# Kernel tuning notes

Hardware: AMD Instinct MI355X
Metric: run time of the kernel (lower is better)

## Reference

```python
import jax, jax.numpy as jnp
import numpy as np
import math

HEADS = 8
EMBED = 512
HEAD_DIM = EMBED // HEADS
N, L = 2, 256


def setup_inputs() -> dict:
    key = jax.random.key(0)
    ks = jax.random.split(key, 16)
    s = 0.05  # weight scale for numerical stability
    inp = {
        "values": jax.random.normal(ks[0], (N, L, EMBED), jnp.float32),
        "keys": jax.random.normal(ks[1], (N, L, EMBED), jnp.float32),
        "query": jax.random.normal(ks[2], (N, L, EMBED), jnp.float32),
        "pos": jax.random.normal(ks[3], (N, L, EMBED), jnp.float32),
        "rel": jax.random.normal(ks[4], (N, L, L, EMBED), jnp.float32),
        "mask": jnp.ones((N, L), jnp.float32),
        "Wv": jax.random.normal(ks[5], (HEAD_DIM, HEAD_DIM), jnp.float32) * s,
        "Wk": jax.random.normal(ks[6], (HEAD_DIM, HEAD_DIM), jnp.float32) * s,
        "Wq": jax.random.normal(ks[7], (HEAD_DIM, HEAD_DIM), jnp.float32) * s,
        "Wpq": jax.random.normal(ks[8], (HEAD_DIM, HEAD_DIM), jnp.float32) * s,
        "Wpk": jax.random.normal(ks[9], (HEAD_DIM, HEAD_DIM), jnp.float32) * s,
        "Wrk": jax.random.normal(ks[10], (HEAD_DIM, HEAD_DIM), jnp.float32) * s,
        "Wrq": jax.random.normal(ks[11], (HEAD_DIM, HEAD_DIM), jnp.float32) * s,
        "Wout": jax.random.normal(ks[12], (EMBED, EMBED), jnp.float32) * s,
        "bout": jnp.zeros((EMBED,), jnp.float32),
    }
    return inp


def reference(values, keys, query, pos, rel, mask, Wv, Wk, Wq, Wpq, Wpk, Wrk, Wrq, Wout, bout):
    n, lq, e = query.shape
    h, d = HEADS, e // HEADS
    # split heads; per-head Linear shares one [d,d] weight (y = x @ W.T)
    v = values.reshape(n, -1, h, d) @ Wv.T
    k = keys.reshape(n, -1, h, d) @ Wk.T
    q = query.reshape(n, lq, h, d) @ Wq.T
    p = pos.reshape(n, lq, h, d)
    r = rel.reshape(n, lq, lq, h, d)
    # mode == 'all': QK + pos-pos + two relative terms
    scores = jnp.einsum('nqhd,nkhd->nhqk', q, k)
    pq = p @ Wpq.T
    pk = p @ Wpk.T
    pos_scores = jnp.einsum('nqhd,nkhd->nhqk', pq, pk)
    rk = r @ Wrk.T
    rq = r @ Wrq.T
    rel1 = jnp.einsum('nqhd,nqkhd->nhqk', q, rk)
    rel2 = jnp.einsum('nqkhd,nkhd->nhqk', rq, k)
    energy = (scores + pos_scores + rel1 + rel2) / math.sqrt(2.0)
    energy = energy + (1.0 - mask)[:, None, None, :] * (-1e9)
    attn = jax.nn.softmax(energy, axis=3)
    out = jnp.einsum('nhqk,nkhd->nqhd', attn, v).reshape(n, lq, e)
    return out @ Wout.T + bout
```

## Files before the change

kernel.cpp:

```cpp
#include <hip/hip_runtime.h>
#include <hip/hip_bf16.h>

#define NB 2
#define L 256
#define H 8
#define D 64
#define E 512
#define NL (NB * L)
#define RSQRT2 0.70710678118654752f

__global__ __launch_bounds__(256) void k0_transpose(
    const float* __restrict__ Wout, float* __restrict__ WoutT,
    const float* __restrict__ Wq, const float* __restrict__ Wk,
    const float* __restrict__ Wv, const float* __restrict__ Wpq,
    const float* __restrict__ Wpk,
    float* __restrict__ WqT, float* __restrict__ WkT, float* __restrict__ WvT,
    float* __restrict__ WpqT, float* __restrict__ WpkT) {
    __shared__ float tile[64][65];
    int t = threadIdx.x;
    int tx = t & 63, ty = t >> 6;
    if (blockIdx.x < 64) {
        int bi = blockIdx.x >> 3;
        int bj = blockIdx.x & 7;
#pragma unroll
        for (int m = 0; m < 16; m++) {
            int el = ty + (m << 2);
            tile[el][tx] = Wout[(size_t)(bi * 64 + el) * E + bj * 64 + tx];
        }
        __syncthreads();
#pragma unroll
        for (int m = 0; m < 16; m++) {
            int cl = ty + (m << 2);
            WoutT[(size_t)(bj * 64 + cl) * E + bi * 64 + tx] = tile[tx][cl];
        }
    } else {
        const float* src;
        float* dst;
        switch (blockIdx.x - 64) {
            case 0: src = Wq;  dst = WqT;  break;
            case 1: src = Wk;  dst = WkT;  break;
            case 2: src = Wv;  dst = WvT;  break;
            case 3: src = Wpq; dst = WpqT; break;
            default: src = Wpk; dst = WpkT; break;
        }
#pragma unroll
        for (int m = 0; m < 16; m++) {
            int r = ty + (m << 2);
            tile[r][tx] = src[(r << 6) + tx];
        }
        __syncthreads();
#pragma unroll
        for (int m = 0; m < 16; m++) {
            int r = ty + (m << 2);
            dst[(r << 6) + tx] = tile[tx][r];
        }
    }
}

__global__ __launch_bounds__(256) void k1_proj(
    const float* __restrict__ values, const float* __restrict__ keys,
    const float* __restrict__ query, const float* __restrict__ pos,
    const float* __restrict__ WqT, const float* __restrict__ WkT,
    const float* __restrict__ WvT, const float* __restrict__ WpqT,
    const float* __restrict__ WpkT, const float* __restrict__ Wrk,
    const float* __restrict__ Wrq,
    float* __restrict__ qv_ws, float* __restrict__ kv_ws,
    float* __restrict__ vv_ws, float* __restrict__ pq_ws,
    float* __restrict__ pk_ws, float* __restrict__ qrk_ws,
    float* __restrict__ krq_ws) {
    __shared__ float xq[E], xk[E], xv[E], xp[E];
    __shared__ float qs[E], ks[E];
    int t = threadIdx.x;
    int nl = blockIdx.x;
    size_t base = (size_t)nl * E;
    for (int j = t; j < E; j += 256) {
        xq[j] = query[base + j];
        xk[j] = keys[base + j];
        xv[j] = values[base + j];
        xp[j] = pos[base + j];
    }
    __syncthreads();
#pragma unroll
    for (int cc = 0; cc < 2; cc++) {
        int c = t + (cc << 8);
        int h = c >> 6, i = c & 63;
        const float* xqh = xq + (h << 6);
        const float* xkh = xk + (h << 6);
        const float* xvh = xv + (h << 6);
        const float* xph = xp + (h << 6);
        float q_c = 0.f, k_c = 0.f, v_c = 0.f, pq_c = 0.f, pk_c = 0.f;
#pragma unroll 8
        for (int j = 0; j < 64; j++) {
            int wi = (j << 6) + i;
            float xqj = xqh[j], xkj = xkh[j], xvj = xvh[j], xpj = xph[j];
            q_c = fmaf(xqj, WqT[wi], q_c);
            k_c = fmaf(xkj, WkT[wi], k_c);
            v_c = fmaf(xvj, WvT[wi], v_c);
            pq_c = fmaf(xpj, WpqT[wi], pq_c);
            pk_c = fmaf(xpj, WpkT[wi], pk_c);
        }
        qv_ws[base + c] = q_c;
        kv_ws[base + c] = k_c;
        vv_ws[base + c] = v_c;
        pq_ws[base + c] = pq_c;
        pk_ws[base + c] = pk_c;
        qs[c] = q_c;
        ks[c] = k_c;
    }
    __syncthreads();
#pragma unroll
    for (int cc = 0; cc < 2; cc++) {
        int c = t + (cc << 8);
        int h = c >> 6, d = c & 63;
        float aq = 0.f, ak = 0.f;
        const float* qh = qs + (h << 6);
        const float* kh = ks + (h << 6);
#pragma unroll 8
        for (int i = 0; i < 64; i++) {
            aq = fmaf(qh[i], Wrk[(i << 6) + d], aq);
            ak = fmaf(kh[i], Wrq[(i << 6) + d], ak);
        }
        qrk_ws[base + c] = aq;
        krq_ws[base + c] = ak;
    }
}

__global__ __launch_bounds__(256) void k2pre(
    const float* __restrict__ qv_ws, const float* __restrict__ kv_ws,
    const float* __restrict__ pq_ws, const float* __restrict__ pk_ws,
    const float* __restrict__ mask, float* __restrict__ e_ws) {
    __shared__ float qs[8 * 64], ps[8 * 64];
    int t = threadIdx.x;
    int b = blockIdx.x;
    int qt = b & 31;
    int h = (b >> 5) & 7;
    int n = b >> 8;
    int nb = n << 8;
    int q0 = qt << 3;
    int k = t;
#pragma unroll
    for (int it = 0; it < 2; it++) {
        int idx = t + (it << 8);
        int q = idx >> 6, d = idx & 63;
        size_t g = (size_t)(nb + q0 + q) * E + (h << 6) + d;
        qs[idx] = qv_ws[g];
        ps[idx] = pq_ws[g];
    }
    __syncthreads();
    const float4* kv4p = (const float4*)(kv_ws + (size_t)(nb + k) * E + (h << 6));
    const float4* pk4p = (const float4*)(pk_ws + (size_t)(nb + k) * E + (h << 6));
    float acc[8];
#pragma unroll
    for (int q = 0; q < 8; q++) acc[q] = 0.f;
#pragma unroll
    for (int d4 = 0; d4 < 16; d4++) {
        float4 kv4 = kv4p[d4];
        float4 pk4 = pk4p[d4];
#pragma unroll
        for (int q = 0; q < 8; q++) {
            float4 q4 = ((const float4*)qs)[(q << 4) + d4];
            float4 p4 = ((const float4*)ps)[(q << 4) + d4];
            float a = acc[q];
            a = fmaf(q4.x, kv4.x, a);
            a = fmaf(q4.y, kv4.y, a);
            a = fmaf(q4.z, kv4.z, a);
            a = fmaf(q4.w, kv4.w, a);
            a = fmaf(p4.x, pk4.x, a);
            a = fmaf(p4.y, pk4.y, a);
            a = fmaf(p4.z, pk4.z, a);
            a = fmaf(p4.w, pk4.w, a);
            acc[q] = a;
        }
    }
    float mk = (1.0f - mask[nb + k]) * (-1e9f);
#pragma unroll
    for (int q = 0; q < 8; q++) {
        e_ws[(size_t)(nb + q0 + q) * (H * L) + (h << 8) + k] = acc[q] * RSQRT2 + mk;
    }
}


#define K2F_LOAD(RR, RK, c_)                                              \
    do {                                                                  \
        _Pragma("unroll") for (int jj = 0; jj < 4; jj++) {                \
            int k_ = ((c_) << 3) + (jj << 1) + rowsel;                    \
            size_t o_ = ((size_t)k_ << 9) + cq;                           \
            RR[jj] = *(const float4*)(relb + o_);                         \
            RK[jj] = *(const float4*)(krqb + o_);                         \
        }                                                                 \
    } while (0)

#define K2F_COMP(RR, RK, c_)                                              \
    do {                                                                  \
        _Pragma("unroll") for (int jj = 0; jj < 4; jj++) {                \
            float wx = qrk4.x + RK[jj].x;                                 \
            float wy = qrk4.y + RK[jj].y;                                 \
            float wz = qrk4.z + RK[jj].z;                                 \
            float ww = qrk4.w + RK[jj].w;                                 \
            float p = RR[jj].x * wx;                                      \
            p = fmaf(RR[jj].y, wy, p);                                    \
            p = fmaf(RR[jj].z, wz, p);                                    \
            p = fmaf(RR[jj].w, ww, p);                                    \
            p += __shfl_down(p, 8, 16);                                   \
            p += __shfl_down(p, 4, 16);                                   \
            p += __shfl_down(p, 2, 16);                                   \
            p += __shfl_down(p, 1, 16);                                   \
            if (sub == 0) {                                               \
                int k_ = ((c_) << 3) + (jj << 1) + rowsel;                \
                r_s[(h << 8) + k_] = p * RSQRT2;                          \
            }                                                             \
        }                                                                 \
    } while (0)

__global__ __launch_bounds__(256, 2) void k2f(
    const float* __restrict__ rel, const float* __restrict__ qrk_ws,
    const float* __restrict__ krq_ws, const float* __restrict__ e_ws,
    const float* __restrict__ vv_ws, float* __restrict__ attn_ws) {
    __shared__ float e_s[H * L];
    __shared__ float r_s[H * L];
    __shared__ float PS[2 * E];
    __shared__ float inv_s[H];
    int t = threadIdx.x;
    int nq = blockIdx.x;
    int n = nq >> 8;

    {
        const float4* src = (const float4*)(e_ws + (size_t)nq * (H * L));
        ((float4*)e_s)[t] = src[t];
        ((float4*)e_s)[t + 256] = src[t + 256];
    }

    int lane128 = t & 127;
    int rowsel = t >> 7;
    int cq = lane128 << 2;
    int h = lane128 >> 4;
    int sub = t & 15;

    const float* relb = rel + (((size_t)nq) << 8) * E;
    const float* krqb = krq_ws + (((size_t)(n << 8))) * E;
    float4 qrk4 = *(const float4*)(qrk_ws + (size_t)nq * E + cq);

    float4 rAr[4], rAk[4], rBr[4], rBk[4];
    K2F_LOAD(rAr, rAk, 0);
#pragma unroll
    for (int c = 0; c < 32; c += 2) {
        K2F_LOAD(rBr, rBk, c + 1);
        K2F_COMP(rAr, rAk, c);
        if (c + 2 < 32) K2F_LOAD(rAr, rAk, c + 2);
        K2F_COMP(rBr, rBk, c + 1);
    }
    __syncthreads();

    {
        int hh = t >> 5;
        int l32 = t & 31;
        float* eh = e_s + (hh << 8);
        const float* rh = r_s + (hh << 8);
        float x[8];
        float m = -INFINITY;
#pragma unroll
        for (int j = 0; j < 8; j++) {
            int idx = l32 + (j << 5);
            x[j] = eh[idx] + rh[idx];
            m = fmaxf(m, x[j]);
        }
#pragma unroll
        for (int off = 16; off > 0; off >>= 1) m = fmaxf(m, __shfl_xor(m, off, 32));
        float s = 0.f;
#pragma unroll
        for (int j = 0; j < 8; j++) {
            int idx = l32 + (j << 5);
            float ev = __expf(x[j] - m);
            eh[idx] = ev;
            s += ev;
        }
#pragma unroll
        for (int off = 16; off > 0; off >>= 1) s += __shfl_xor(s, off, 32);
        if (l32 == 0) inv_s[hh] = 1.0f / s;
    }
    __syncthreads();

    {
        int c4 = (t & 127) << 2;
        int kseg = t >> 7;
        int h1 = c4 >> 6;
        const float* eh = e_s + (h1 << 8) + (kseg << 7);
        const float* vb = vv_ws + ((size_t)((n << 8) + (kseg << 7))) * E + c4;
        float4 acc = {0.f, 0.f, 0.f, 0.f};
#pragma unroll 16
        for (int k = 0; k < 128; k++) {
            float ev = eh[k];
            float4 v4 = *(const float4*)(vb + ((size_t)k << 9));
            acc.x = fmaf(ev, v4.x, acc.x);
            acc.y = fmaf(ev, v4.y, acc.y);
            acc.z = fmaf(ev, v4.z, acc.z);
            acc.w = fmaf(ev, v4.w, acc.w);
        }
        *(float4*)(PS + kseg * E + c4) = acc;
    }
    __syncthreads();

    {
        float v0 = PS[t] + PS[E + t];
        attn_ws[(size_t)nq * E + t] = v0 * inv_s[t >> 6];
        float v1 = PS[256 + t] + PS[E + 256 + t];
        attn_ws[(size_t)nq * E + 256 + t] = v1 * inv_s[(256 + t) >> 6];
    }
}

__global__ __launch_bounds__(512) void k3_out(const float* __restrict__ attn_ws,
                                              const float* __restrict__ WoutT,
                                              const float* __restrict__ bout,
                                              float* __restrict__ out) {
    __shared__ float As[4 * E];
    int t = threadIdx.x;
    int r0 = blockIdx.x << 2;
    for (int j = t; j < 4 * E; j += 512) As[j] = attn_ws[(size_t)r0 * E + j];
    __syncthreads();
    float b0 = bout[t];
    float a0 = b0, a1 = b0, a2 = b0, a3 = b0;
#pragma unroll 8
    for (int c = 0; c < E; c++) {
        float w = WoutT[((size_t)c << 9) + t];
        a0 = fmaf(As[c], w, a0);
        a1 = fmaf(As[E + c], w, a1);
        a2 = fmaf(As[2 * E + c], w, a2);
        a3 = fmaf(As[3 * E + c], w, a3);
    }
    out[(size_t)(r0 + 0) * E + t] = a0;
    out[(size_t)(r0 + 1) * E + t] = a1;
    out[(size_t)(r0 + 2) * E + t] = a2;
    out[(size_t)(r0 + 3) * E + t] = a3;
}

extern "C" void kernel_launch(void* const* d_in, const int* in_sizes, int n_in,
                              void* d_out, int out_size, void* d_ws, size_t ws_size,
                              hipStream_t stream) {
    const float* values = (const float*)d_in[0];
    const float* keys = (const float*)d_in[1];
    const float* query = (const float*)d_in[2];
    const float* pos = (const float*)d_in[3];
    const float* rel = (const float*)d_in[4];
    const float* mask = (const float*)d_in[5];
    const float* Wv = (const float*)d_in[6];
    const float* Wk = (const float*)d_in[7];
    const float* Wq = (const float*)d_in[8];
    const float* Wpq = (const float*)d_in[9];
    const float* Wpk = (const float*)d_in[10];
    const float* Wrk = (const float*)d_in[11];
    const float* Wrq = (const float*)d_in[12];
    const float* Wout = (const float*)d_in[13];
    const float* bout = (const float*)d_in[14];
    float* out = (float*)d_out;

    float* ws = (float*)d_ws;
    const size_t SZ = (size_t)NL * E;
    float* qv_ws = ws + 0 * SZ;
    float* kv_ws = ws + 1 * SZ;
    float* vv_ws = ws + 2 * SZ;
    float* pq_ws = ws + 3 * SZ;
    float* pk_ws = ws + 4 * SZ;
    float* qrk_ws = ws + 5 * SZ;
    float* krq_ws = ws + 6 * SZ;
    float* attn_ws = ws + 7 * SZ;
    float* WoutT = ws + 8 * SZ;
    float* e_ws = ws + 9 * SZ;
    float* WqT = e_ws + (size_t)NL * (H * L);
    float* WkT = WqT + 4096;
    float* WvT = WkT + 4096;
    float* WpqT = WvT + 4096;
    float* WpkT = WpqT + 4096;

    k0_transpose<<<69, 256, 0, stream>>>(Wout, WoutT, Wq, Wk, Wv, Wpq, Wpk,
                                         WqT, WkT, WvT, WpqT, WpkT);
    k1_proj<<<NL, 256, 0, stream>>>(values, keys, query, pos, WqT, WkT, WvT,
                                    WpqT, WpkT, Wrk, Wrq, qv_ws, kv_ws, vv_ws,
                                    pq_ws, pk_ws, qrk_ws, krq_ws);
    k2pre<<<512, 256, 0, stream>>>(qv_ws, kv_ws, pq_ws, pk_ws, mask, e_ws);
    k2f<<<512, 256, 0, stream>>>(rel, qrk_ws, krq_ws, e_ws, vv_ws, attn_ws);
    k3_out<<<NL / 4, 512, 0, stream>>>(attn_ws, WoutT, bout, out);
}
```

Baseline: 503.7 us.

## Register-block k1 projections over four outputs, two tokens per block; deepen k2f prefetch

k1_proj now handles two tokens per block. Each thread computes four adjacent output columns using float4 weight loads and padded LDS rows, which cuts the number of weight-load instructions and the block count by half. Separately, k2f's rel/krq prefetch buffers grow from 4 to 8 rows per stage, so more memory requests are in flight over the dominant rel stream. This raises register pressure in k2f (32 float4 buffers), which could spill or reduce occupancy under launch_bounds(256,2).

```diff
diff --git a/kernel.cpp b/kernel.cpp
--- a/kernel.cpp
+++ b/kernel.cpp
@@ -57,6 +57,8 @@
     }
 }
 
+#define XS 68
+
 __global__ __launch_bounds__(256) void k1_proj(
     const float* __restrict__ values, const float* __restrict__ keys,
     const float* __restrict__ query, const float* __restrict__ pos,
@@ -68,60 +70,98 @@
     float* __restrict__ vv_ws, float* __restrict__ pq_ws,
     float* __restrict__ pk_ws, float* __restrict__ qrk_ws,
     float* __restrict__ krq_ws) {
-    __shared__ float xq[E], xk[E], xv[E], xp[E];
-    __shared__ float qs[E], ks[E];
+    __shared__ float x_lds[4][2][8 * XS];
+    __shared__ float qk_lds[2][2][8 * XS];
     int t = threadIdx.x;
-    int nl = blockIdx.x;
-    size_t base = (size_t)nl * E;
-    for (int j = t; j < E; j += 256) {
-        xq[j] = query[base + j];
-        xk[j] = keys[base + j];
-        xv[j] = values[base + j];
-        xp[j] = pos[base + j];
-    }
-    __syncthreads();
-#pragma unroll
-    for (int cc = 0; cc < 2; cc++) {
-        int c = t + (cc << 8);
-        int h = c >> 6, i = c & 63;
-        const float* xqh = xq + (h << 6);
-        const float* xkh = xk + (h << 6);
-        const float* xvh = xv + (h << 6);
-        const float* xph = xp + (h << 6);
-        float q_c = 0.f, k_c = 0.f, v_c = 0.f, pq_c = 0.f, pk_c = 0.f;
+    int tok0 = blockIdx.x << 1;
+
+    {
+        int tk = t >> 7;
+        int quad = t & 127;
+        int hh = quad >> 4;
+        int li = quad & 15;
+        size_t g = (size_t)(tok0 + tk) * E + (quad << 2);
+        float4 vq = *(const float4*)(query + g);
+        float4 vk = *(const float4*)(keys + g);
+        float4 vv = *(const float4*)(values + g);
+        float4 vp = *(const float4*)(pos + g);
+        int o = hh * XS + (li << 2);
+        *(float4*)&x_lds[0][tk][o] = vq;
+        *(float4*)&x_lds[1][tk][o] = vk;
+        *(float4*)&x_lds[2][tk][o] = vv;
+        *(float4*)&x_lds[3][tk][o] = vp;
+    }
+    __syncthreads();
+
+    int tk = t >> 7;
+    int quad = t & 127;
+    int h = quad >> 4;
+    int li = quad & 15;
+    const float* xq = &x_lds[0][tk][h * XS];
+    const float* xk = &x_lds[1][tk][h * XS];
+    const float* xv = &x_lds[2][tk][h * XS];
+    const float* xp = &x_lds[3][tk][h * XS];
+    const float4* wq4 = (const float4*)WqT + li;
+    const float4* wk4 = (const float4*)WkT + li;
+    const float4* wv4 = (const float4*)WvT + li;
+    const float4* wpq4 = (const float4*)WpqT + li;
+    const float4* wpk4 = (const float4*)WpkT + li;
+
+    float4 aq = {0, 0, 0, 0}, ak = {0, 0, 0, 0}, av = {0, 0, 0, 0};
+    float4 apq = {0, 0, 0, 0}, apk = {0, 0, 0, 0};
 #pragma unroll 8
-        for (int j = 0; j < 64; j++) {
-            int wi = (j << 6) + i;
-            float xqj = xqh[j], xkj = xkh[j], xvj = xvh[j], xpj = xph[j];
-            q_c = fmaf(xqj, WqT[wi], q_c);
-            k_c = fmaf(xkj, WkT[wi], k_c);
-            v_c = fmaf(xvj, WvT[wi], v_c);
-            pq_c = fmaf(xpj, WpqT[wi], pq_c);
-            pk_c = fmaf(xpj, WpkT[wi], pk_c);
-        }
-        qv_ws[base + c] = q_c;
-        kv_ws[base + c] = k_c;
-        vv_ws[base + c] = v_c;
-        pq_ws[base + c] = pq_c;
-        pk_ws[base + c] = pk_c;
-        qs[c] = q_c;
-        ks[c] = k_c;
-    }
-    __syncthreads();
-#pragma unroll
-    for (int cc = 0; cc < 2; cc++) {
-        int c = t + (cc << 8);
-        int h = c >> 6, d = c & 63;
-        float aq = 0.f, ak = 0.f;
-        const float* qh = qs + (h << 6);
-        const float* kh = ks + (h << 6);
+    for (int j = 0; j < 64; j++) {
+        float xqj = xq[j], xkj = xk[j], xvj = xv[j], xpj = xp[j];
+        float4 w;
+        w = wq4[j << 4];
+        aq.x = fmaf(xqj, w.x, aq.x); aq.y = fmaf(xqj, w.y, aq.y);
+        aq.z = fmaf(xqj, w.z, aq.z); aq.w = fmaf(xqj, w.w, aq.w);
+        w = wk4[j << 4];
+        ak.x = fmaf(xkj, w.x, ak.x); ak.y = fmaf(xkj, w.y, ak.y);
+        ak.z = fmaf(xkj, w.z, ak.z); ak.w = fmaf(xkj, w.w, ak.w);
+        w = wv4[j << 4];
+        av.x = fmaf(xvj, w.x, av.x); av.y = fmaf(xvj, w.y, av.y);
+        av.z = fmaf(xvj, w.z, av.z); av.w = fmaf(xvj, w.w, av.w);
+        w = wpq4[j << 4];
+        apq.x = fmaf(xpj, w.x, apq.x); apq.y = fmaf(xpj, w.y, apq.y);
+        apq.z = fmaf(xpj, w.z, apq.z); apq.w = fmaf(xpj, w.w, apq.w);
+        w = wpk4[j << 4];
+        apk.x = fmaf(xpj, w.x, apk.x); apk.y = fmaf(xpj, w.y, apk.y);
+        apk.z = fmaf(xpj, w.z, apk.z); apk.w = fmaf(xpj, w.w, apk.w);
+    }
+    {
+        size_t g = (size_t)(tok0 + tk) * E + (h << 6) + (li << 2);
+        *(float4*)(qv_ws + g) = aq;
+        *(float4*)(kv_ws + g) = ak;
+        *(float4*)(vv_ws + g) = av;
+        *(float4*)(pq_ws + g) = apq;
+        *(float4*)(pk_ws + g) = apk;
+        int o = h * XS + (li << 2);
+        *(float4*)&qk_lds[0][tk][o] = aq;
+        *(float4*)&qk_lds[1][tk][o] = ak;
+    }
+    __syncthreads();
+
+    {
+        const float* qh = &qk_lds[0][tk][h * XS];
+        const float* kh = &qk_lds[1][tk][h * XS];
+        const float4* wrk4 = (const float4*)Wrk + li;
+        const float4* wrq4 = (const float4*)Wrq + li;
+        float4 ark = {0, 0, 0, 0}, arq = {0, 0, 0, 0};
 #pragma unroll 8
         for (int i = 0; i < 64; i++) {
-            aq = fmaf(qh[i], Wrk[(i << 6) + d], aq);
-            ak = fmaf(kh[i], Wrq[(i << 6) + d], ak);
-        }
-        qrk_ws[base + c] = aq;
-        krq_ws[base + c] = ak;
+            float qi = qh[i], ki = kh[i];
+            float4 w;
+            w = wrk4[i << 4];
+            ark.x = fmaf(qi, w.x, ark.x); ark.y = fmaf(qi, w.y, ark.y);
+            ark.z = fmaf(qi, w.z, ark.z); ark.w = fmaf(qi, w.w, ark.w);
+            w = wrq4[i << 4];
+            arq.x = fmaf(ki, w.x, arq.x); arq.y = fmaf(ki, w.y, arq.y);
+            arq.z = fmaf(ki, w.z, arq.z); arq.w = fmaf(ki, w.w, arq.w);
+        }
+        size_t g = (size_t)(tok0 + tk) * E + (h << 6) + (li << 2);
+        *(float4*)(qrk_ws + g) = ark;
+        *(float4*)(krq_ws + g) = arq;
     }
 }
 
@@ -179,20 +219,18 @@
     }
 }
 
-
-#define K2F_LOAD(RR, RK, c_)                                              \
+#define K2F_LOAD(RR, RK, b_)                                              \
     do {                                                                  \
-        _Pragma("unroll") for (int jj = 0; jj < 4; jj++) {                \
-            int k_ = ((c_) << 3) + (jj << 1) + rowsel;                    \
-            size_t o_ = ((size_t)k_ << 9) + cq;                           \
-            RR[jj] = *(const float4*)(relb + o_);                         \
-            RK[jj] = *(const float4*)(krqb + o_);                         \
+        _Pragma("unroll") for (int jj = 0; jj < 8; jj++) {                \
+            int k_ = ((b_) << 4) + (jj << 1) + rowsel;                    \
+            RR[jj] = *(const float4*)(relb + ((size_t)k_ << 9) + cq);     \
+            RK[jj] = *(const float4*)(krqb + ((size_t)k_ << 9) + cq);     \
         }                                                                 \
     } while (0)
 
-#define K2F_COMP(RR, RK, c_)                                              \
+#define K2F_COMP(RR, RK, b_)                                              \
     do {                                                                  \
-        _Pragma("unroll") for (int jj = 0; jj < 4; jj++) {                \
+        _Pragma("unroll") for (int jj = 0; jj < 8; jj++) {                \
             float wx = qrk4.x + RK[jj].x;                                 \
             float wy = qrk4.y + RK[jj].y;                                 \
             float wz = qrk4.z + RK[jj].z;                                 \
@@ -206,7 +244,7 @@
             p += __shfl_down(p, 2, 16);                                   \
             p += __shfl_down(p, 1, 16);                                   \
             if (sub == 0) {                                               \
-                int k_ = ((c_) << 3) + (jj << 1) + rowsel;                \
+                int k_ = ((b_) << 4) + (jj << 1) + rowsel;                \
                 r_s[(h << 8) + k_] = p * RSQRT2;                          \
             }                                                             \
         }                                                                 \
@@ -240,14 +278,14 @@
     const float* krqb = krq_ws + (((size_t)(n << 8))) * E;
     float4 qrk4 = *(const float4*)(qrk_ws + (size_t)nq * E + cq);
 
-    float4 rAr[4], rAk[4], rBr[4], rBk[4];
+    float4 rAr[8], rAk[8], rBr[8], rBk[8];
     K2F_LOAD(rAr, rAk, 0);
 #pragma unroll
-    for (int c = 0; c < 32; c += 2) {
-        K2F_LOAD(rBr, rBk, c + 1);
-        K2F_COMP(rAr, rAk, c);
-        if (c + 2 < 32) K2F_LOAD(rAr, rAk, c + 2);
-        K2F_COMP(rBr, rBk, c + 1);
+    for (int b = 0; b < 16; b += 2) {
+        K2F_LOAD(rBr, rBk, b + 1);
+        K2F_COMP(rAr, rAk, b);
+        if (b + 2 < 16) K2F_LOAD(rAr, rAk, b + 2);
+        K2F_COMP(rBr, rBk, b + 1);
     }
     __syncthreads();
 
@@ -373,9 +411,10 @@
 
     k0_transpose<<<69, 256, 0, stream>>>(Wout, WoutT, Wq, Wk, Wv, Wpq, Wpk,
                                          WqT, WkT, WvT, WpqT, WpkT);
-    k1_proj<<<NL, 256, 0, stream>>>(values, keys, query, pos, WqT, WkT, WvT,
-                                    WpqT, WpkT, Wrk, Wrq, qv_ws, kv_ws, vv_ws,
-                                    pq_ws, pk_ws, qrk_ws, krq_ws);
+    k1_proj<<<NL / 2, 256, 0, stream>>>(values, keys, query, pos, WqT, WkT,
+                                        WvT, WpqT, WpkT, Wrk, Wrq, qv_ws,
+                                        kv_ws, vv_ws, pq_ws, pk_ws, qrk_ws,
+                                        krq_ws);
     k2pre<<<512, 256, 0, stream>>>(qv_ws, kv_ws, pq_ws, pk_ws, mask, e_ws);
     k2f<<<512, 256, 0, stream>>>(rel, qrk_ws, krq_ws, e_ws, vv_ws, attn_ws);
     k3_out<<<NL / 4, 512, 0, stream>>>(attn_ws, WoutT, bout, out);
```

After: 533.5 us. +5.9%, slower.
